# Performance work log

Measured on AMD Instinct MI355X. Metric: run time of the kernel, lower is better.

## Reference

```python
import jax, jax.numpy as jnp
import numpy as np

# Static module config (must match init_kwargs / input_specs)
C, HEADS, POINTS, LEVELS = 256, 8, 8, 2
H, W = 128, 128           # BEV grid per agent/level
NQ = H * W                # num_query = H*W
DH = C // HEADS           # per-head dim


def setup_inputs() -> dict:
    key = jax.random.key(0)
    ks = jax.random.split(key, 12)
    s = 0.02
    return {
        "query": jax.random.normal(ks[0], (1, NQ, C), jnp.float32),
        "query_pos": jax.random.normal(ks[1], (1, NQ, C), jnp.float32),
        "value": jax.random.normal(ks[2], (LEVELS, NQ, C), jnp.float32),
        "reference_points": jax.random.uniform(ks[3], (1, NQ, LEVELS, 2), jnp.float32),
        "spatial_shapes": jnp.full((LEVELS, 2), H, dtype=jnp.int32),
        "W_off": jax.random.normal(ks[4], (C, LEVELS * HEADS * POINTS * 2), jnp.float32) * s,
        "b_off": jax.random.normal(ks[5], (LEVELS * HEADS * POINTS * 2,), jnp.float32) * s,
        "W_attn": jax.random.normal(ks[6], (C, LEVELS * HEADS * POINTS), jnp.float32) * s,
        "b_attn": jax.random.normal(ks[7], (LEVELS * HEADS * POINTS,), jnp.float32) * s,
        "W_val": jax.random.normal(ks[8], (C, C), jnp.float32) * s,
        "b_val": jax.random.normal(ks[9], (C,), jnp.float32) * s,
        "W_out": jax.random.normal(ks[10], (C, C), jnp.float32) * s,
        "b_out": jax.random.normal(ks[11], (C,), jnp.float32) * s,
    }


def _bilinear(img, x, y):
    """grid_sample-style bilinear, align_corners=False, zero padding.
    img: (H, W, D); x, y: (...) pixel-space coords. Returns (..., D)."""
    Hh, Ww = img.shape[0], img.shape[1]
    x0f, y0f = jnp.floor(x), jnp.floor(y)
    x0, y0 = x0f.astype(jnp.int32), y0f.astype(jnp.int32)
    x1, y1 = x0 + 1, y0 + 1
    wx1, wy1 = x - x0f, y - y0f
    wx0, wy0 = 1.0 - wx1, 1.0 - wy1

    def gather(yy, xx):
        valid = (yy >= 0) & (yy < Hh) & (xx >= 0) & (xx < Ww)
        g = img[jnp.clip(yy, 0, Hh - 1), jnp.clip(xx, 0, Ww - 1)]
        return jnp.where(valid[..., None], g, 0.0)

    return (gather(y0, x0) * (wy0 * wx0)[..., None]
            + gather(y0, x1) * (wy0 * wx1)[..., None]
            + gather(y1, x0) * (wy1 * wx0)[..., None]
            + gather(y1, x1) * (wy1 * wx1)[..., None])


_sample_heads = jax.vmap(_bilinear, in_axes=(0, 0, 0))  # over heads


def reference(query, query_pos, value, reference_points, spatial_shapes,
              W_off, b_off, W_attn, b_attn, W_val, b_val, W_out, b_out):
    identity = query                                        # (1, NQ, C)
    q = (query + query_pos)[0]                              # (NQ, C), bs=1

    v = value @ W_val + b_val                               # (L, NQ, C)
    v = v.reshape(LEVELS, H, W, HEADS, DH)                  # per-level feature maps

    off = (q @ W_off + b_off).reshape(NQ, HEADS, LEVELS, POINTS, 2)
    attn = (q @ W_attn + b_attn).reshape(NQ, HEADS, LEVELS * POINTS)
    attn = jax.nn.softmax(attn, axis=-1).reshape(NQ, HEADS, LEVELS, POINTS)

    # offset_normalizer = (W, H) per level
    norm = jnp.stack([spatial_shapes[:, 1], spatial_shapes[:, 0]], -1).astype(q.dtype)  # (L, 2)
    # sampling_locations in normalized [0,1] coords: (NQ, HEADS, LEVELS, POINTS, 2)
    loc = reference_points[0][:, None, :, None, :] + off / norm[None, None, :, None, :]

    out = jnp.zeros((NQ, HEADS, DH), dtype=q.dtype)
    for l in range(LEVELS):
        img_l = jnp.transpose(v[l], (2, 0, 1, 3))           # (HEADS, H, W, DH)
        # align_corners=False: px = x_norm * W - 0.5
        xl = jnp.transpose(loc[:, :, l, :, 0], (1, 0, 2)) * W - 0.5  # (HEADS, NQ, POINTS)
        yl = jnp.transpose(loc[:, :, l, :, 1], (1, 0, 2)) * H - 0.5
        sampled = _sample_heads(img_l, xl, yl)              # (HEADS, NQ, POINTS, DH)
        out = out + jnp.einsum('hqpd,qhp->qhd', sampled, attn[:, :, l, :])

    out = out.reshape(NQ, C) @ W_out + b_out                # (NQ, C)
    return out[None] + identity                             # dropout is identity (eval / p=0)
```

## Files before the change

kernel.cpp:

```cpp
#include <hip/hip_runtime.h>
#include <hip/hip_bf16.h>
#include <math.h>

#define NQ     16384
#define CDIM   256
#define NHEADS 8
#define NPTS   8
#define NLVL   2
#define HH     128
#define WWID   128
#define DHEAD  32
#define NCAT   384

typedef __bf16 bf16_t;
typedef __bf16 bf16x8 __attribute__((ext_vector_type(8)));
typedef float  f32x4  __attribute__((ext_vector_type(4)));

typedef __attribute__((address_space(1))) const uint32_t gau32;
typedef __attribute__((address_space(3))) uint32_t lau32;

__device__ __forceinline__ bf16_t f2b(float f) { return (bf16_t)f; }

__global__ __launch_bounds__(256) void wtrans_all_k(const float* __restrict__ W_val,
                                                    const float* __restrict__ W_off,
                                                    const float* __restrict__ W_attn,
                                                    const float* __restrict__ W_out,
                                                    bf16_t* __restrict__ Wt_val,
                                                    bf16_t* __restrict__ Wt_qa,
                                                    bf16_t* __restrict__ Wt_out) {
    const int b = blockIdx.x;
    const float* W; bf16_t* Wt; int N, base;
    if (b < 256)      { W = W_val;  Wt = Wt_val;            N = 256; base = 0;   }
    else if (b < 512) { W = W_off;  Wt = Wt_qa;             N = 256; base = 256; }
    else if (b < 640) { W = W_attn; Wt = Wt_qa + 256 * 256; N = 128; base = 512; }
    else              { W = W_out;  Wt = Wt_out;            N = 256; base = 640; }
    int i = (b - base) * 256 + threadIdx.x;
    int n = i >> 8, k = i & 255;
    if (n >= N) return;
    Wt[i] = f2b(W[(size_t)k * N + n]);
}

template <int A_MODE, bool OUT_BF16, bool ADD_SRC, bool PERM_V>
__device__ __forceinline__ void gemm_body(bf16_t (&As)[128][64], bf16_t (&Bs)[128][64],
                                          int bidx, int bidy,
                                          const void* __restrict__ Aptr,
                                          const void* __restrict__ Aptr2,
                                          const bf16_t* __restrict__ Bt,
                                          const float* __restrict__ bias,
                                          const float* __restrict__ bias2,
                                          int Nsplit,
                                          const float* __restrict__ addsrc,
                                          void* __restrict__ Cout,
                                          int N, int K) {
    const int tid  = threadIdx.x;
    const int wave = tid >> 6;
    const int lane = tid & 63;
    const int rowBase = bidy * 128;
    const int colBase = bidx * 128;
    const int wm = (wave & 1) * 64;
    const int wn = (wave >> 1) * 64;
    const int fr = lane & 15;
    const int fq = lane >> 4;

    f32x4 acc[4][4] = {};

    const int lrow = lane >> 3;
    const int lcol = (lane & 7) * 8;

    for (int k0 = 0; k0 < K; k0 += 64) {
        __syncthreads();
        if (A_MODE != 0) {
            const int r = tid >> 1, kc = (tid & 1) * 32;
            const float* ap = (const float*)Aptr + (size_t)(rowBase + r) * K + k0 + kc;
            const float* ap2 = (A_MODE == 2)
                ? (const float*)Aptr2 + (size_t)(rowBase + r) * K + k0 + kc : nullptr;
            bf16_t* dst = &As[r][kc];
#pragma unroll
            for (int u = 0; u < 4; ++u) {
                float4 f0 = *reinterpret_cast<const float4*>(ap + u * 8);
                float4 f1 = *reinterpret_cast<const float4*>(ap + u * 8 + 4);
                if (A_MODE == 2) {
                    float4 g0 = *reinterpret_cast<const float4*>(ap2 + u * 8);
                    float4 g1 = *reinterpret_cast<const float4*>(ap2 + u * 8 + 4);
                    f0.x += g0.x; f0.y += g0.y; f0.z += g0.z; f0.w += g0.w;
                    f1.x += g1.x; f1.y += g1.y; f1.z += g1.z; f1.w += g1.w;
                }
                bf16x8 bv;
                bv[0] = f2b(f0.x); bv[1] = f2b(f0.y); bv[2] = f2b(f0.z); bv[3] = f2b(f0.w);
                bv[4] = f2b(f1.x); bv[5] = f2b(f1.y); bv[6] = f2b(f1.z); bv[7] = f2b(f1.w);
                *reinterpret_cast<bf16x8*>(dst + u * 8) = bv;
            }
        } else {
            const bf16_t* Abf = (const bf16_t*)Aptr;
#pragma unroll
            for (int t = 0; t < 4; ++t) {
                const bf16_t* src =
                    Abf + (size_t)(rowBase + wave * 32 + t * 8 + lrow) * K + k0 + lcol;
                __builtin_amdgcn_global_load_lds((gau32*)src,
                                                 (lau32*)&As[wave * 32 + t * 8][0],
                                                 16, 0, 0);
            }
        }
#pragma unroll
        for (int t = 0; t < 4; ++t) {
            const bf16_t* src =
                Bt + (size_t)(colBase + wave * 32 + t * 8 + lrow) * K + k0 + lcol;
            __builtin_amdgcn_global_load_lds((gau32*)src,
                                             (lau32*)&Bs[wave * 32 + t * 8][0],
                                             16, 0, 0);
        }
        __syncthreads();
#pragma unroll
        for (int ks = 0; ks < 2; ++ks) {
            bf16x8 af[4], bfr[4];
#pragma unroll
            for (int i = 0; i < 4; ++i)
                af[i] = *reinterpret_cast<const bf16x8*>(&As[wm + i * 16 + fr][ks * 32 + fq * 8]);
#pragma unroll
            for (int j = 0; j < 4; ++j)
                bfr[j] = *reinterpret_cast<const bf16x8*>(&Bs[wn + j * 16 + fr][ks * 32 + fq * 8]);
#pragma unroll
            for (int i = 0; i < 4; ++i)
#pragma unroll
                for (int j = 0; j < 4; ++j)
                    acc[i][j] = __builtin_amdgcn_mfma_f32_16x16x32_bf16(af[i], bfr[j],
                                                                        acc[i][j], 0, 0, 0);
        }
    }

#pragma unroll
    for (int j = 0; j < 4; ++j) {
        const int col = colBase + wn + j * 16 + fr;
        const float bv = (col < Nsplit) ? bias[col] : bias2[col - Nsplit];
#pragma unroll
        for (int i = 0; i < 4; ++i) {
#pragma unroll
            for (int r = 0; r < 4; ++r) {
                const int row = rowBase + wm + i * 16 + fq * 4 + r;
                float vv = acc[i][j][r] + bv;
                if (ADD_SRC) vv += addsrc[(size_t)row * N + col];
                if (PERM_V) {
                    const int l = row >> 14, cell = row & 16383;
                    const size_t dst =
                        (((size_t)(l * NHEADS + (col >> 5)) * NQ + cell) << 5) + (col & 31);
                    ((bf16_t*)Cout)[dst] = f2b(vv);
                } else if (OUT_BF16) {
                    ((bf16_t*)Cout)[(size_t)row * N + col] = f2b(vv);
                } else {
                    ((float*)Cout)[(size_t)row * N + col] = vv;
                }
            }
        }
    }
}

__global__ __launch_bounds__(256, 3) void fused_proj_k(const float* __restrict__ value,
                                                       const float* __restrict__ query,
                                                       const float* __restrict__ query_pos,
                                                       const bf16_t* __restrict__ Wt_val,
                                                       const bf16_t* __restrict__ Wt_qa,
                                                       const float* __restrict__ b_val,
                                                       const float* __restrict__ b_off,
                                                       const float* __restrict__ b_attn,
                                                       bf16_t* __restrict__ v2,
                                                       float* __restrict__ cbuf) {
    __shared__ __align__(16) bf16_t As[128][64];
    __shared__ __align__(16) bf16_t Bs[128][64];
    const int b = blockIdx.x;
    if (b < 512) {
        gemm_body<1, true, false, true>(As, Bs, b & 1, b >> 1, value, nullptr,
                                        Wt_val, b_val, b_val, 256, nullptr, v2,
                                        CDIM, CDIM);
    } else {
        const int b2 = b - 512;
        gemm_body<2, false, false, false>(As, Bs, b2 % 3, b2 / 3, query, query_pos,
                                          Wt_qa, b_off, b_attn, 256, nullptr, cbuf,
                                          NCAT, CDIM);
    }
}

__global__ __launch_bounds__(256, 3) void outproj_k(const bf16_t* __restrict__ tmp,
                                                    const bf16_t* __restrict__ Wt_out,
                                                    const float* __restrict__ b_out,
                                                    const float* __restrict__ query,
                                                    float* __restrict__ out) {
    __shared__ __align__(16) bf16_t As[128][64];
    __shared__ __align__(16) bf16_t Bs[128][64];
    const int b = blockIdx.x;
    gemm_body<0, false, true, false>(As, Bs, b & 1, b >> 1, tmp, nullptr,
                                     Wt_out, b_out, b_out, 256, query, out,
                                     CDIM, CDIM);
}

__global__ __launch_bounds__(256) void sample_k(const bf16_t* __restrict__ v2,
                                                const float* __restrict__ cbuf,
                                                const float* __restrict__ refp,
                                                bf16_t* __restrict__ tmp) {
    const int b    = blockIdx.x;
    const int h    = b & 7;
    const int qblk = b >> 3;
    const int tid  = threadIdx.x;
    const int qloc = tid >> 2;
    const int ck   = tid & 3;
    const int q    = qblk * 64 + qloc;

    const float* qrow = cbuf + (size_t)q * NCAT;
    const float4 rp = *reinterpret_cast<const float4*>(refp + (size_t)q * 4);

    const float* attp = qrow + 256 + h * 16;
    float4 A0 = *reinterpret_cast<const float4*>(attp);
    float4 A1 = *reinterpret_cast<const float4*>(attp + 4);
    float4 A2 = *reinterpret_cast<const float4*>(attp + 8);
    float4 A3 = *reinterpret_cast<const float4*>(attp + 12);
    float e[16] = {A0.x, A0.y, A0.z, A0.w, A1.x, A1.y, A1.z, A1.w,
                   A2.x, A2.y, A2.z, A2.w, A3.x, A3.y, A3.z, A3.w};
    float m = e[0];
#pragma unroll
    for (int i = 1; i < 16; ++i) m = fmaxf(m, e[i]);
    float s = 0.f;
#pragma unroll
    for (int i = 0; i < 16; ++i) { e[i] = __expf(e[i] - m); s += e[i]; }
    const float inv = 1.f / s;
#pragma unroll
    for (int i = 0; i < 16; ++i) e[i] *= inv;

    float acc[8] = {0.f, 0.f, 0.f, 0.f, 0.f, 0.f, 0.f, 0.f};

#pragma unroll
    for (int l = 0; l < NLVL; ++l) {
        const float bx = (l == 0 ? rp.x : rp.z) * (float)WWID - 0.5f;
        const float by = (l == 0 ? rp.y : rp.w) * (float)HH - 0.5f;
        const bf16_t* base = v2 + ((size_t)(l * NHEADS + h) * NQ) * DHEAD + ck * 8;
        const float* offp  = qrow + h * 32 + l * 16;

        float4 o0 = *reinterpret_cast<const float4*>(offp);
        float4 o1 = *reinterpret_cast<const float4*>(offp + 4);
        float4 o2 = *reinterpret_cast<const float4*>(offp + 8);
        float4 o3 = *reinterpret_cast<const float4*>(offp + 12);
        const float ox[8] = {o0.x, o0.z, o1.x, o1.z, o2.x, o2.z, o3.x, o3.z};
        const float oy[8] = {o0.y, o0.w, o1.y, o1.w, o2.y, o2.w, o3.y, o3.w};

#pragma unroll
        for (int p = 0; p < NPTS; ++p) {
            const float px = bx + ox[p];
            const float py = by + oy[p];
            const float w  = e[l * 8 + p];
            const float x0f = floorf(px), y0f = floorf(py);
            const int x0 = (int)x0f, y0 = (int)y0f;
            const float wx1 = px - x0f, wy1 = py - y0f;
            const float wx0 = 1.f - wx1, wy0 = 1.f - wy1;
            const bool vx0 = (unsigned)x0 < (unsigned)WWID;
            const bool vx1 = (unsigned)(x0 + 1) < (unsigned)WWID;
            const bool vy0 = (unsigned)y0 < (unsigned)HH;
            const bool vy1 = (unsigned)(y0 + 1) < (unsigned)HH;
            const int xc0 = min(max(x0, 0), WWID - 1);
            const int xc1 = min(max(x0 + 1, 0), WWID - 1);
            const int yc0 = min(max(y0, 0), HH - 1);
            const int yc1 = min(max(y0 + 1, 0), HH - 1);
            const bf16_t* r0 = base + yc0 * (WWID * DHEAD);
            const bf16_t* r1 = base + yc1 * (WWID * DHEAD);
            bf16x8 v00 = *reinterpret_cast<const bf16x8*>(r0 + xc0 * DHEAD);
            bf16x8 v10 = *reinterpret_cast<const bf16x8*>(r0 + xc1 * DHEAD);
            bf16x8 v01 = *reinterpret_cast<const bf16x8*>(r1 + xc0 * DHEAD);
            bf16x8 v11 = *reinterpret_cast<const bf16x8*>(r1 + xc1 * DHEAD);
            const float w00 = (vx0 & vy0) ? w * wx0 * wy0 : 0.f;
            const float w10 = (vx1 & vy0) ? w * wx1 * wy0 : 0.f;
            const float w01 = (vx0 & vy1) ? w * wx0 * wy1 : 0.f;
            const float w11 = (vx1 & vy1) ? w * wx1 * wy1 : 0.f;
#pragma unroll
            for (int i = 0; i < 8; ++i) {
                acc[i] = fmaf(w00, (float)v00[i], acc[i]);
                acc[i] = fmaf(w10, (float)v10[i], acc[i]);
                acc[i] = fmaf(w01, (float)v01[i], acc[i]);
                acc[i] = fmaf(w11, (float)v11[i], acc[i]);
            }
        }
    }

    bf16x8 ov;
#pragma unroll
    for (int i = 0; i < 8; ++i) ov[i] = f2b(acc[i]);
    *reinterpret_cast<bf16x8*>(tmp + (size_t)q * CDIM + h * DHEAD + ck * 8) = ov;
}

extern "C" void kernel_launch(void* const* d_in, const int* in_sizes, int n_in,
                              void* d_out, int out_size, void* d_ws, size_t ws_size,
                              hipStream_t stream) {
    const float* query     = (const float*)d_in[0];
    const float* query_pos = (const float*)d_in[1];
    const float* value     = (const float*)d_in[2];
    const float* refp      = (const float*)d_in[3];
    const float* W_off  = (const float*)d_in[5];
    const float* b_off  = (const float*)d_in[6];
    const float* W_attn = (const float*)d_in[7];
    const float* b_attn = (const float*)d_in[8];
    const float* W_val  = (const float*)d_in[9];
    const float* b_val  = (const float*)d_in[10];
    const float* W_out  = (const float*)d_in[11];
    const float* b_out  = (const float*)d_in[12];
    float* out = (float*)d_out;

    char* ws = (char*)d_ws;
    bf16_t* v2      = (bf16_t*)(ws);
    float*  cbuf    = (float*)(ws + 16777216);
    bf16_t* tmp     = (bf16_t*)(ws + 41943040);
    bf16_t* Wt_val  = (bf16_t*)(ws + 50331648);
    bf16_t* Wt_qa   = (bf16_t*)(ws + 50462720);
    bf16_t* Wt_out  = (bf16_t*)(ws + 50659328);

    wtrans_all_k<<<896, 256, 0, stream>>>(W_val, W_off, W_attn, W_out,
                                          Wt_val, Wt_qa, Wt_out);
    fused_proj_k<<<896, 256, 0, stream>>>(value, query, query_pos,
                                          Wt_val, Wt_qa, b_val, b_off, b_attn,
                                          v2, cbuf);
    sample_k<<<2048, 256, 0, stream>>>(v2, cbuf, refp, tmp);
    outproj_k<<<256, 256, 0, stream>>>(tmp, Wt_out, b_out, query, out);
}
```

Measured before the change: 216.8 us.

## XOR-swizzle GEMM LDS tiles and remap block order for L2 locality

Applies an XOR swizzle to the 16-byte chunks of the shared-memory A/B tiles, both on the global_load_lds and register-store paths and on the MFMA fragment reads, to cut LDS bank conflicts from the row-strided 128-byte rows. It also remaps block indices so groups of 8 row tiles iterate across column tiles together, aiming to improve L2 reuse of A rows. This adds index arithmetic, and the swizzle must stay consistent between writes and reads to remain correct.

```diff
diff --git a/kernel.cpp b/kernel.cpp
--- a/kernel.cpp
+++ b/kernel.cpp
@@ -65,16 +65,15 @@
     f32x4 acc[4][4] = {};
 
     const int lrow = lane >> 3;
-    const int lcol = (lane & 7) * 8;
+    const int scol = ((lane & 7) ^ lrow) * 8;
 
     for (int k0 = 0; k0 < K; k0 += 64) {
         __syncthreads();
         if (A_MODE != 0) {
-            const int r = tid >> 1, kc = (tid & 1) * 32;
-            const float* ap = (const float*)Aptr + (size_t)(rowBase + r) * K + k0 + kc;
+            const int r = tid >> 1, c = tid & 1;
+            const float* ap = (const float*)Aptr + (size_t)(rowBase + r) * K + k0 + c * 32;
             const float* ap2 = (A_MODE == 2)
-                ? (const float*)Aptr2 + (size_t)(rowBase + r) * K + k0 + kc : nullptr;
-            bf16_t* dst = &As[r][kc];
+                ? (const float*)Aptr2 + (size_t)(rowBase + r) * K + k0 + c * 32 : nullptr;
 #pragma unroll
             for (int u = 0; u < 4; ++u) {
                 float4 f0 = *reinterpret_cast<const float4*>(ap + u * 8);
@@ -88,14 +87,15 @@
                 bf16x8 bv;
                 bv[0] = f2b(f0.x); bv[1] = f2b(f0.y); bv[2] = f2b(f0.z); bv[3] = f2b(f0.w);
                 bv[4] = f2b(f1.x); bv[5] = f2b(f1.y); bv[6] = f2b(f1.z); bv[7] = f2b(f1.w);
-                *reinterpret_cast<bf16x8*>(dst + u * 8) = bv;
+                const int gp = ((c * 4 + u) ^ (r & 7)) * 8;
+                *reinterpret_cast<bf16x8*>(&As[r][gp]) = bv;
             }
         } else {
             const bf16_t* Abf = (const bf16_t*)Aptr;
 #pragma unroll
             for (int t = 0; t < 4; ++t) {
                 const bf16_t* src =
-                    Abf + (size_t)(rowBase + wave * 32 + t * 8 + lrow) * K + k0 + lcol;
+                    Abf + (size_t)(rowBase + wave * 32 + t * 8 + lrow) * K + k0 + scol;
                 __builtin_amdgcn_global_load_lds((gau32*)src,
                                                  (lau32*)&As[wave * 32 + t * 8][0],
                                                  16, 0, 0);
@@ -104,7 +104,7 @@
 #pragma unroll
         for (int t = 0; t < 4; ++t) {
             const bf16_t* src =
-                Bt + (size_t)(colBase + wave * 32 + t * 8 + lrow) * K + k0 + lcol;
+                Bt + (size_t)(colBase + wave * 32 + t * 8 + lrow) * K + k0 + scol;
             __builtin_amdgcn_global_load_lds((gau32*)src,
                                              (lau32*)&Bs[wave * 32 + t * 8][0],
                                              16, 0, 0);
@@ -112,13 +112,14 @@
         __syncthreads();
 #pragma unroll
         for (int ks = 0; ks < 2; ++ks) {
+            const int gk = ((ks * 4 + fq) ^ (fr & 7)) * 8;
             bf16x8 af[4], bfr[4];
 #pragma unroll
             for (int i = 0; i < 4; ++i)
-                af[i] = *reinterpret_cast<const bf16x8*>(&As[wm + i * 16 + fr][ks * 32 + fq * 8]);
+                af[i] = *reinterpret_cast<const bf16x8*>(&As[wm + i * 16 + fr][gk]);
 #pragma unroll
             for (int j = 0; j < 4; ++j)
-                bfr[j] = *reinterpret_cast<const bf16x8*>(&Bs[wn + j * 16 + fr][ks * 32 + fq * 8]);
+                bfr[j] = *reinterpret_cast<const bf16x8*>(&Bs[wn + j * 16 + fr][gk]);
 #pragma unroll
             for (int i = 0; i < 4; ++i)
 #pragma unroll
@@ -168,12 +169,16 @@
     __shared__ __align__(16) bf16_t Bs[128][64];
     const int b = blockIdx.x;
     if (b < 512) {
-        gemm_body<1, true, false, true>(As, Bs, b & 1, b >> 1, value, nullptr,
+        const int bidy = (b >> 4) * 8 + (b & 7);
+        const int bidx = (b >> 3) & 1;
+        gemm_body<1, true, false, true>(As, Bs, bidx, bidy, value, nullptr,
                                         Wt_val, b_val, b_val, 256, nullptr, v2,
                                         CDIM, CDIM);
     } else {
         const int b2 = b - 512;
-        gemm_body<2, false, false, false>(As, Bs, b2 % 3, b2 / 3, query, query_pos,
+        const int bidy = (b2 / 24) * 8 + (b2 & 7);
+        const int bidx = (b2 >> 3) % 3;
+        gemm_body<2, false, false, false>(As, Bs, bidx, bidy, query, query_pos,
                                           Wt_qa, b_off, b_attn, 256, nullptr, cbuf,
                                           NCAT, CDIM);
     }
@@ -187,7 +192,9 @@
     __shared__ __align__(16) bf16_t As[128][64];
     __shared__ __align__(16) bf16_t Bs[128][64];
     const int b = blockIdx.x;
-    gemm_body<0, false, true, false>(As, Bs, b & 1, b >> 1, tmp, nullptr,
+    const int bidy = (b >> 4) * 8 + (b & 7);
+    const int bidx = (b >> 3) & 1;
+    gemm_body<0, false, true, false>(As, Bs, bidx, bidy, tmp, nullptr,
                                      Wt_out, b_out, b_out, 256, query, out,
                                      CDIM, CDIM);
 }
```

Result: faster. 211.3 us (-2.5%).
